# Kernel tuning notes

Measured on AMD Instinct MI355X. Metric: run time of the kernel, lower is better.

The kernel has to match this reference:

```python
import jax, jax.numpy as jnp
import numpy as np

S, B, D = 2048, 2, 768
H = 12
DK = D // H
DFF = 3072
EPS = 1e-5


def _layernorm(x, g, b):
    mu = jnp.mean(x, axis=-1, keepdims=True)
    var = jnp.mean(jnp.square(x - mu), axis=-1, keepdims=True)
    return (x - mu) * jax.lax.rsqrt(var + EPS) * g + b


def setup_inputs() -> dict:
    key = jax.random.key(0)
    ks = jax.random.split(key, 12)
    s = 0.02
    return {
        "x": jax.random.normal(ks[0], (S, B, D), jnp.float32),
        "wq": jax.random.normal(ks[1], (D, D), jnp.float32) * s,
        "bq": jnp.zeros((D,), jnp.float32),
        "wk": jax.random.normal(ks[2], (D, D), jnp.float32) * s,
        "bk": jnp.zeros((D,), jnp.float32),
        "wv": jax.random.normal(ks[3], (D, D), jnp.float32) * s,
        "bv": jnp.zeros((D,), jnp.float32),
        "wo": jax.random.normal(ks[4], (D, D), jnp.float32) * s,
        "bo": jnp.zeros((D,), jnp.float32),
        "g1": jnp.ones((D,), jnp.float32),
        "b1": jnp.zeros((D,), jnp.float32),
        "g2": jnp.ones((D,), jnp.float32),
        "b2": jnp.zeros((D,), jnp.float32),
        "w1": jax.random.normal(ks[5], (DFF, D), jnp.float32) * s,
        "bb1": jnp.zeros((DFF,), jnp.float32),
        "w2": jax.random.normal(ks[6], (D, DFF), jnp.float32) * s,
        "bb2": jnp.zeros((D,), jnp.float32),
    }


def reference(x, wq, bq, wk, bk, wv, bv, wo, bo, g1, b1, g2, b2, w1, bb1, w2, bb2):
    scale = 1.0 / np.sqrt(DK)
    # --- pre-norm MHA ---
    z = _layernorm(x, g1, b1)                      # [S,B,D]
    q = (z @ wq.T + bq).reshape(S, B, H, DK)
    k = (z @ wk.T + bk).reshape(S, B, H, DK)
    v = (z @ wv.T + bv).reshape(S, B, H, DK)
    scores = jnp.einsum('ibhd,jbhd->ijbh', q, k) * scale  # [S,S,B,H]
    attn = jax.nn.softmax(scores, axis=1)                  # softmax over keys
    ctx = jnp.einsum('ijbh,jbhd->ibhd', attn, v).reshape(S, B, D)
    a = ctx @ wo.T + bo
    x = x + a
    # --- pre-norm FFN (ELU) ---
    z = _layernorm(x, g2, b2)
    h = jax.nn.elu(z @ w1.T + bb1)
    a = h @ w2.T + bb2
    return x + a
```

## Files before the change

### kernel.cpp

```cpp
#include <hip/hip_runtime.h>
#include <hip/hip_bf16.h>
#include <math.h>

#define S_LEN   2048
#define B_SZ    2
#define D_MODEL 768
#define N_HEADS 12
#define DFF     3072
#define N_TOK   4096
#define EPS     1e-5f
#define QKV_N   2304
#define SLOG2E  0.18033688011112042f
#define NSPLIT  2
#define NTILE   (S_LEN / 64 / NSPLIT)

typedef __attribute__((ext_vector_type(8))) short short8;
typedef __attribute__((ext_vector_type(4))) float f32x4;
typedef unsigned long long u64;
typedef unsigned short u16;
typedef unsigned u32;

__device__ __forceinline__ void gload16(const void* g, void* l) {
    __builtin_amdgcn_global_load_lds(
        (const __attribute__((address_space(1))) void*)g,
        (__attribute__((address_space(3))) void*)l, 16, 0, 0);
}
__device__ __forceinline__ u16 f2bf(float x) {
    union { float f; unsigned u; } c; c.f = x;
    unsigned r = c.u + 0x7FFF + ((c.u >> 16) & 1);
    return (u16)(r >> 16);
}
__device__ __forceinline__ float bf2f(u16 u) {
    union { unsigned u; float f; } c; c.u = ((unsigned)u) << 16; return c.f;
}
__device__ __forceinline__ float fast_exp2(float x) {
    float r; asm("v_exp_f32 %0, %1" : "=v"(r) : "v"(x)); return r;
}

__global__ __launch_bounds__(256) void cvt_all(
    const float* __restrict__ wq, const float* __restrict__ wk,
    const float* __restrict__ wv, const float* __restrict__ wo,
    const float* __restrict__ w1, const float* __restrict__ w2,
    u16* __restrict__ dst)
{
    const int W = 147456;
    int i = blockIdx.x * 256 + threadIdx.x;
    const float* src; int off;
    if      (i <     W) { src = wq; off = 0;     }
    else if (i < 2 * W) { src = wk; off = W;     }
    else if (i < 3 * W) { src = wv; off = 2 * W; }
    else if (i < 4 * W) { src = wo; off = 3 * W; }
    else if (i < 8 * W) { src = w1; off = 4 * W; }
    else                { src = w2; off = 8 * W; }
    float4 v = ((const float4*)src)[i - off];
    union { u16 u[4]; u64 ll; } o;
    o.u[0] = f2bf(v.x); o.u[1] = f2bf(v.y); o.u[2] = f2bf(v.z); o.u[3] = f2bf(v.w);
    ((u64*)dst)[i] = o.ll;
}

__global__ __launch_bounds__(256) void concat_bias(
    const float* __restrict__ bq, const float* __restrict__ bk,
    const float* __restrict__ bv, float* __restrict__ d)
{
    int i = blockIdx.x * 256 + threadIdx.x;
    if (i < 768) d[i] = bq[i];
    else if (i < 1536) d[i] = bk[i - 768];
    else d[i] = bv[i - 1536];
}

__global__ __launch_bounds__(256) void ln_kernel(
    const float* __restrict__ x, const float* __restrict__ g,
    const float* __restrict__ b, u16* __restrict__ z)
{
    int row = blockIdx.x;
    const float* xr = x + (size_t)row * D_MODEL;
    u16* zr = z + (size_t)row * D_MODEL;
    int t = threadIdx.x;
    float loc[3];
    float s1 = 0.f, s2 = 0.f;
#pragma unroll
    for (int i = 0; i < 3; ++i) {
        float v = xr[t + 256 * i];
        loc[i] = v; s1 += v; s2 += v * v;
    }
#pragma unroll
    for (int off = 32; off > 0; off >>= 1) {
        s1 += __shfl_down(s1, off);
        s2 += __shfl_down(s2, off);
    }
    __shared__ float r1[4], r2[4];
    __shared__ float mu_s, is_s;
    int wave = t >> 6, lane = t & 63;
    if (lane == 0) { r1[wave] = s1; r2[wave] = s2; }
    __syncthreads();
    if (t == 0) {
        float a = r1[0] + r1[1] + r1[2] + r1[3];
        float c = r2[0] + r2[1] + r2[2] + r2[3];
        float mu = a * (1.f / D_MODEL);
        float var = c * (1.f / D_MODEL) - mu * mu;
        mu_s = mu; is_s = rsqrtf(var + EPS);
    }
    __syncthreads();
    float mu = mu_s, istd = is_s;
#pragma unroll
    for (int i = 0; i < 3; ++i) {
        int c = t + 256 * i;
        zr[c] = f2bf((loc[i] - mu) * istd * g[c] + b[c]);
    }
}

__global__ __launch_bounds__(256) void ln_fuse(
    const float* __restrict__ x, const u16* __restrict__ p0,
    const u16* __restrict__ p1, const float* __restrict__ bres,
    const float* __restrict__ g, const float* __restrict__ b,
    float* __restrict__ xout, u16* __restrict__ z)
{
    int row = blockIdx.x;
    const float* xr = x + (size_t)row * D_MODEL;
    const u16* p0r = p0 + (size_t)row * D_MODEL;
    const u16* p1r = p1 + (size_t)row * D_MODEL;
    int t = threadIdx.x;
    float loc[3];
    float s1 = 0.f, s2 = 0.f;
#pragma unroll
    for (int i = 0; i < 3; ++i) {
        int c = t + 256 * i;
        float v = xr[c] + bf2f(p0r[c]) + bf2f(p1r[c]) + bres[c];
        loc[i] = v; s1 += v; s2 += v * v;
    }
#pragma unroll
    for (int off = 32; off > 0; off >>= 1) {
        s1 += __shfl_down(s1, off);
        s2 += __shfl_down(s2, off);
    }
    __shared__ float r1[4], r2[4];
    __shared__ float mu_s, is_s;
    int wave = t >> 6, lane = t & 63;
    if (lane == 0) { r1[wave] = s1; r2[wave] = s2; }
    __syncthreads();
    if (t == 0) {
        float a = r1[0] + r1[1] + r1[2] + r1[3];
        float c = r2[0] + r2[1] + r2[2] + r2[3];
        float mu = a * (1.f / D_MODEL);
        float var = c * (1.f / D_MODEL) - mu * mu;
        mu_s = mu; is_s = rsqrtf(var + EPS);
    }
    __syncthreads();
    float mu = mu_s, istd = is_s;
    float* xo = xout + (size_t)row * D_MODEL;
    u16* zr = z + (size_t)row * D_MODEL;
#pragma unroll
    for (int i = 0; i < 3; ++i) {
        int c = t + 256 * i;
        xo[c] = loc[i];
        zr[c] = f2bf((loc[i] - mu) * istd * g[c] + b[c]);
    }
}

template <int MODE>
__global__ __launch_bounds__(256) void gemm_mfma(
    const u16* __restrict__ A, const u16* __restrict__ W,
    const float* __restrict__ bias, void* __restrict__ outp,
    u16* __restrict__ vt, int Ncols, int K, int lda, int ldw, int koff)
{
    __shared__ short AsB[3][128 * 32];
    __shared__ short BsB[3][128 * 32];

    const int t = threadIdx.x;
    const int lane = t & 63, w = t >> 6;
    const int wr = w >> 1, wc = w & 1;
    const int row0 = blockIdx.y * 128, col0 = blockIdx.x * 128;
    const int fr = lane & 15, fg = lane >> 4;

    if (MODE == 4) {
        A += (size_t)blockIdx.z * koff;
        W += (size_t)blockIdx.z * koff;
    }

    int o0 = w * 1024 + lane * 16;
    int r0s = o0 >> 6,          sl0 = (o0 >> 4) & 3;
    int r1s = (o0 + 4096) >> 6, sl1 = ((o0 + 4096) >> 4) & 3;
    int ss0 = sl0 ^ ((r0s >> 1) & 3);
    int ss1 = sl1 ^ ((r1s >> 1) & 3);
    const u16* Asrc0 = A + (size_t)(row0 + r0s) * lda + ss0 * 8;
    const u16* Asrc1 = A + (size_t)(row0 + r1s) * lda + ss1 * 8;
    const u16* Bsrc0 = W + (size_t)(col0 + r0s) * ldw + ss0 * 8;
    const u16* Bsrc1 = W + (size_t)(col0 + r1s) * ldw + ss1 * 8;
    const int od0 = w * 1024, od1 = w * 1024 + 4096;

    f32x4 acc[4][4] = {};
    const int nt = K / 32;

    auto stage = [&](int c, int k0) {
        gload16(Asrc0 + k0, (char*)AsB[c] + od0);
        gload16(Asrc1 + k0, (char*)AsB[c] + od1);
        gload16(Bsrc0 + k0, (char*)BsB[c] + od0);
        gload16(Bsrc1 + k0, (char*)BsB[c] + od1);
    };

    stage(0, 0);
    stage(1, 32);

    for (int tt = 0; tt < nt; ++tt) {
        if (tt + 1 < nt)
            asm volatile("s_waitcnt vmcnt(4)\n\ts_barrier" ::: "memory");
        else
            asm volatile("s_waitcnt vmcnt(0)\n\ts_barrier" ::: "memory");
        if (tt + 2 < nt) stage((tt + 2) % 3, (tt + 2) * 32);

        const char* As = (const char*)AsB[tt % 3];
        const char* Bs = (const char*)BsB[tt % 3];
        short8 af[4], bfr[4];
#pragma unroll
        for (int m = 0; m < 4; ++m) {
            int r = wr * 64 + m * 16 + fr;
            af[m] = *(const short8*)(As + r * 64 + ((fg ^ ((r >> 1) & 3)) << 4));
        }
#pragma unroll
        for (int n = 0; n < 4; ++n) {
            int r = wc * 64 + n * 16 + fr;
            bfr[n] = *(const short8*)(Bs + r * 64 + ((fg ^ ((r >> 1) & 3)) << 4));
        }
#pragma unroll
        for (int m = 0; m < 4; ++m)
#pragma unroll
            for (int n = 0; n < 4; ++n)
                acc[m][n] = __builtin_amdgcn_mfma_f32_16x16x32_bf16(
                    af[m], bfr[n], acc[m][n], 0, 0, 0);
    }

    u16* pout16 = nullptr;
    if (MODE == 4) pout16 = blockIdx.z ? vt : (u16*)outp;

#pragma unroll
    for (int m = 0; m < 4; ++m) {
        int rbase = row0 + wr * 64 + m * 16 + fg * 4;
#pragma unroll
        for (int n = 0; n < 4; ++n) {
            int col = col0 + wc * 64 + n * 16 + fr;
            float bv = (MODE == 4) ? 0.f : bias[col];
            if (MODE == 1 && col >= 1536) {
                int cc = col - 1536, hh = cc >> 6, dk = cc & 63;
                int s_a = rbase >> 1;
                float v0 = acc[m][n][0] + bv, v1 = acc[m][n][1] + bv;
                float v2 = acc[m][n][2] + bv, v3 = acc[m][n][3] + bv;
                unsigned lo = (unsigned)f2bf(v0) | ((unsigned)f2bf(v2) << 16);
                unsigned hi = (unsigned)f2bf(v1) | ((unsigned)f2bf(v3) << 16);
                *(unsigned*)&vt[((size_t)hh * 64 + dk) * 2048 + s_a] = lo;
                *(unsigned*)&vt[((size_t)(N_HEADS + hh) * 64 + dk) * 2048 + s_a] = hi;
            } else {
#pragma unroll
                for (int r = 0; r < 4; ++r) {
                    int row = rbase + r;
                    float v = acc[m][n][r] + bv;
                    if (MODE == 3) {
                        v = v > 0.f ? v : (fast_exp2(v * 1.44269504f) - 1.f);
                        ((u16*)outp)[(size_t)row * Ncols + col] = f2bf(v);
                    } else if (MODE == 4) {
                        pout16[(size_t)row * 768 + col] = f2bf(v);
                    } else {
                        if (col < 768) v *= SLOG2E;
                        ((u16*)outp)[(size_t)row * QKV_N + col] = f2bf(v);
                    }
                }
            }
        }
    }
}

__global__ __launch_bounds__(256) void reduce_add(
    const u16* __restrict__ p0, const u16* __restrict__ p1,
    const float* __restrict__ bias, const float* __restrict__ res,
    float* __restrict__ out)
{
    int i = blockIdx.x * 256 + threadIdx.x;
    int col4 = i % (D_MODEL / 4);
    u64 a = ((const u64*)p0)[i];
    u64 c = ((const u64*)p1)[i];
    float4 o = ((const float4*)res)[i];
    float4 bb = ((const float4*)bias)[col4];
    o.x += bf2f((u16)a)         + bf2f((u16)c)         + bb.x;
    o.y += bf2f((u16)(a >> 16)) + bf2f((u16)(c >> 16)) + bb.y;
    o.z += bf2f((u16)(a >> 32)) + bf2f((u16)(c >> 32)) + bb.z;
    o.w += bf2f((u16)(a >> 48)) + bf2f((u16)(c >> 48)) + bb.w;
    ((float4*)out)[i] = o;
}

__global__ __launch_bounds__(256) void attn_mfma(
    const u16* qkv, const u16* __restrict__ vt,
    u16* op0, u16* __restrict__ op1, float2* __restrict__ mlp)
{
    __shared__ short KsB[2][64 * 64];
    __shared__ short VtB[2][64 * 64];
    __shared__ short PsB[4][16 * 64];

    const int t = threadIdx.x, lane = t & 63, w = t >> 6;
    const int fr = lane & 15, fg = lane >> 4;
    const int fg4 = fg * 4;
    const int qb = blockIdx.x, bh = blockIdx.y, zid = blockIdx.z;
    const int b = bh / N_HEADS, h = bh % N_HEADS;

    short8 qf[2];
    {
        int srow = qb * 64 + w * 16 + fr;
        size_t tok = (size_t)srow * B_SZ + b;
#pragma unroll
        for (int s = 0; s < 2; ++s)
            qf[s] = *(const short8*)(qkv + tok * QKV_N + h * 64 + s * 32 + fg * 8);
    }

    const short8 ones8 = { (short)0x3F80, (short)0x3F80, (short)0x3F80, (short)0x3F80,
                           (short)0x3F80, (short)0x3F80, (short)0x3F80, (short)0x3F80 };

    float m2 = -1e30f;
    f32x4 l_acc = {};
    f32x4 O[4] = {};

    int o0 = w * 1024 + lane * 16;
    int r0 = o0 >> 7,          sl0 = (o0 >> 4) & 7;
    int r1 = (o0 + 4096) >> 7, sl1 = ((o0 + 4096) >> 4) & 7;
    int ss0 = sl0 ^ (r0 & 7), ss1 = sl1 ^ (r1 & 7);
    const u16* kbase = qkv + 768 + h * 64;
    const u16* vtb = vt + (size_t)bh * 64 * S_LEN;
    const int od0 = w * 1024, od1 = w * 1024 + 4096;
    char* Pw = (char*)PsB[w];

    auto stageKV = [&](int c, int kb) {
        gload16(kbase + ((size_t)(kb * 64 + r0) * B_SZ + b) * QKV_N + ss0 * 8, (char*)KsB[c] + od0);
        gload16(kbase + ((size_t)(kb * 64 + r1) * B_SZ + b) * QKV_N + ss1 * 8, (char*)KsB[c] + od1);
        gload16(vtb + (size_t)r0 * S_LEN + kb * 64 + ss0 * 8, (char*)VtB[c] + od0);
        gload16(vtb + (size_t)r1 * S_LEN + kb * 64 + ss1 * 8, (char*)VtB[c] + od1);
    };

    const int kb0 = zid * NTILE;
    stageKV(0, kb0);

    for (int it = 0; it < NTILE; ++it) {
        __syncthreads();
        if (it + 1 < NTILE) stageKV((it + 1) & 1, kb0 + it + 1);
        const char* Ks  = (const char*)KsB[it & 1];
        const char* Vts = (const char*)VtB[it & 1];

        f32x4 sacc[4] = {};
        __builtin_amdgcn_s_setprio(1);
#pragma unroll
        for (int f = 0; f < 4; ++f) {
            int r = f * 16 + fr;
#pragma unroll
            for (int s = 0; s < 2; ++s) {
                int slot = (s * 4 + fg) ^ (r & 7);
                short8 kf = *(const short8*)(Ks + r * 128 + slot * 16);
                sacc[f] = __builtin_amdgcn_mfma_f32_16x16x32_bf16(kf, qf[s], sacc[f], 0, 0, 0);
            }
        }
        __builtin_amdgcn_s_setprio(0);

        float p[16];
        float mx = -1e30f;
#pragma unroll
        for (int f = 0; f < 4; ++f)
#pragma unroll
            for (int r = 0; r < 4; ++r) {
                float vv = sacc[f][r];
                p[f * 4 + r] = vv;
                mx = fmaxf(mx, vv);
            }
        mx = fmaxf(mx, __shfl_xor(mx, 16));
        mx = fmaxf(mx, __shfl_xor(mx, 32));

        if (!__all(mx - m2 <= 8.f)) {
            float mnew = fmaxf(m2, mx);
            float alpha = fast_exp2(m2 - mnew);
            m2 = mnew;
            float a0 = __shfl(alpha, fg4 + 0), a1 = __shfl(alpha, fg4 + 1);
            float a2 = __shfl(alpha, fg4 + 2), a3 = __shfl(alpha, fg4 + 3);
#pragma unroll
            for (int n = 0; n < 4; ++n) {
                O[n][0] *= a0; O[n][1] *= a1; O[n][2] *= a2; O[n][3] *= a3;
            }
            l_acc[0] *= a0; l_acc[1] *= a1; l_acc[2] *= a2; l_acc[3] *= a3;
        }

#pragma unroll
        for (int i = 0; i < 16; ++i)
            p[i] = fast_exp2(p[i] - m2);

#pragma unroll
        for (int f = 0; f < 4; ++f) {
            u32 u0, u1;
            asm("v_cvt_pk_bf16_f32 %0, %1, %2" : "=v"(u0) : "v"(p[4 * f + 0]), "v"(p[4 * f + 1]));
            asm("v_cvt_pk_bf16_f32 %0, %1, %2" : "=v"(u1) : "v"(p[4 * f + 2]), "v"(p[4 * f + 3]));
            int slot = (f * 2 + (fg >> 1)) ^ (fr & 7);
            uint2 uu; uu.x = u0; uu.y = u1;
            *(uint2*)(Pw + fr * 128 + slot * 16 + (fg & 1) * 8) = uu;
        }
        asm volatile("s_waitcnt lgkmcnt(0)" ::: "memory");
        __builtin_amdgcn_sched_barrier(0);

        __builtin_amdgcn_s_setprio(1);
#pragma unroll
        for (int s = 0; s < 2; ++s) {
            int pslot = (s * 4 + fg) ^ (fr & 7);
            short8 pf = *(const short8*)(Pw + fr * 128 + pslot * 16);
            l_acc = __builtin_amdgcn_mfma_f32_16x16x32_bf16(pf, ones8, l_acc, 0, 0, 0);
#pragma unroll
            for (int n = 0; n < 4; ++n) {
                int vrow = n * 16 + fr;
                int vslot = (s * 4 + fg) ^ (vrow & 7);
                short8 vf = *(const short8*)(Vts + vrow * 128 + vslot * 16);
                O[n] = __builtin_amdgcn_mfma_f32_16x16x32_bf16(pf, vf, O[n], 0, 0, 0);
            }
        }
        __builtin_amdgcn_s_setprio(0);
    }

    float mm0 = __shfl(m2, fg4 + 0), mm1 = __shfl(m2, fg4 + 1);
    float mm2 = __shfl(m2, fg4 + 2), mm3 = __shfl(m2, fg4 + 3);
    int srow = qb * 64 + w * 16 + fg4;
    size_t tok0 = (size_t)srow * B_SZ + b;
    u16* op = zid ? op1 : op0;
    const int ld = zid ? 768 : QKV_N;
#pragma unroll
    for (int n = 0; n < 4; ++n) {
        int col = h * 64 + n * 16 + fr;
        op[(tok0 + 0) * ld + col] = f2bf(O[n][0]);
        op[(tok0 + 2) * ld + col] = f2bf(O[n][1]);
        op[(tok0 + 4) * ld + col] = f2bf(O[n][2]);
        op[(tok0 + 6) * ld + col] = f2bf(O[n][3]);
    }
    if (fr == 0) {
        float2* mlz = mlp + (size_t)zid * (N_TOK * N_HEADS);
        mlz[(tok0 + 0) * N_HEADS + h] = make_float2(mm0, l_acc[0]);
        mlz[(tok0 + 2) * N_HEADS + h] = make_float2(mm1, l_acc[1]);
        mlz[(tok0 + 4) * N_HEADS + h] = make_float2(mm2, l_acc[2]);
        mlz[(tok0 + 6) * N_HEADS + h] = make_float2(mm3, l_acc[3]);
    }
}

__global__ __launch_bounds__(256) void combine_attn(
    const u16* __restrict__ op0, const u16* op1,
    const float2* __restrict__ ml, u16* ctx)
{
    int i = blockIdx.x * 256 + threadIdx.x;
    int tok = i / 192, c4 = i % 192, h = c4 >> 4;
    float2 q0 = ml[tok * N_HEADS + h];
    float2 q1 = ml[N_TOK * N_HEADS + tok * N_HEADS + h];
    float m = fmaxf(q0.x, q1.x);
    float a0 = fast_exp2(q0.x - m), a1 = fast_exp2(q1.x - m);
    float inv = 1.f / (a0 * q0.y + a1 * q1.y);
    a0 *= inv; a1 *= inv;
    u64 o0 = *(const u64*)(op0 + (size_t)tok * QKV_N + c4 * 4);
    u64 o1 = *(const u64*)(op1 + (size_t)tok * 768 + c4 * 4);
    union { u16 u[4]; u64 ll; } r;
#pragma unroll
    for (int j = 0; j < 4; ++j)
        r.u[j] = f2bf(a0 * bf2f((u16)(o0 >> (16 * j))) +
                      a1 * bf2f((u16)(o1 >> (16 * j))));
    *(u64*)(ctx + (size_t)tok * 768 + c4 * 4) = r.ll;
}

extern "C" void kernel_launch(void* const* d_in, const int* in_sizes, int n_in,
                              void* d_out, int out_size, void* d_ws, size_t ws_size,
                              hipStream_t stream)
{
    (void)in_sizes; (void)n_in; (void)out_size; (void)ws_size;
    const float* x   = (const float*)d_in[0];
    const float* wq  = (const float*)d_in[1];
    const float* bq  = (const float*)d_in[2];
    const float* wk  = (const float*)d_in[3];
    const float* bk  = (const float*)d_in[4];
    const float* wv  = (const float*)d_in[5];
    const float* bv  = (const float*)d_in[6];
    const float* wo  = (const float*)d_in[7];
    const float* bo  = (const float*)d_in[8];
    const float* g1  = (const float*)d_in[9];
    const float* b1  = (const float*)d_in[10];
    const float* g2  = (const float*)d_in[11];
    const float* b2  = (const float*)d_in[12];
    const float* w1  = (const float*)d_in[13];
    const float* bb1 = (const float*)d_in[14];
    const float* w2  = (const float*)d_in[15];
    const float* bb2 = (const float*)d_in[16];
    float* out = (float*)d_out;

    const size_t ND = (size_t)N_TOK * D_MODEL;
    char* p = (char*)d_ws;
    u16* z    = (u16*)p;
    p += ND * 2;
    u16* qkv  = (u16*)p;
    u16* hbuf = (u16*)p;
    p += (size_t)N_TOK * QKV_N * 2;
    u16* vtb  = (u16*)p;
    p += (size_t)B_SZ * N_HEADS * 64 * S_LEN * 2;
    u16* wqkvb = (u16*)p;
    p += (size_t)QKV_N * D_MODEL * 2;
    u16* wob   = (u16*)p; p += (size_t)D_MODEL * D_MODEL * 2;
    u16* w1b   = (u16*)p; p += (size_t)DFF * D_MODEL * 2;
    u16* w2b   = (u16*)p; p += (size_t)D_MODEL * DFF * 2;
    float* biasqkv = (float*)p;

    u16* aop0 = qkv + 1536;
    u16* aop1 = z;
    float2* aml = (float2*)wqkvb;
    u16* wop0 = qkv;
    u16* wop1 = qkv + ND;
    u16* fp0  = z;
    u16* fp1  = wqkvb;

    dim3 blk(256);

    cvt_all<<<6912, blk, 0, stream>>>(wq, wk, wv, wo, w1, w2, wqkvb);
    concat_bias<<<9, blk, 0, stream>>>(bq, bk, bv, biasqkv);

    ln_kernel<<<N_TOK, blk, 0, stream>>>(x, g1, b1, z);
    gemm_mfma<1><<<dim3(QKV_N / 128, N_TOK / 128), blk, 0, stream>>>(
        z, wqkvb, biasqkv, qkv, vtb, QKV_N, D_MODEL, D_MODEL, D_MODEL, 0);
    attn_mfma<<<dim3(S_LEN / 64, B_SZ * N_HEADS, NSPLIT), blk, 0, stream>>>(
        qkv, vtb, aop0, aop1, aml);
    combine_attn<<<(int)(ND / 4 / 256), blk, 0, stream>>>(aop0, aop1, aml, z);
    gemm_mfma<4><<<dim3(D_MODEL / 128, N_TOK / 128, 2), blk, 0, stream>>>(
        z, wob, nullptr, wop0, wop1, D_MODEL, 384, D_MODEL, D_MODEL, 384);
    ln_fuse<<<N_TOK, blk, 0, stream>>>(x, wop0, wop1, bo, g2, b2, out, z);
    gemm_mfma<3><<<dim3(DFF / 128, N_TOK / 128), blk, 0, stream>>>(
        z, w1b, bb1, hbuf, nullptr, DFF, D_MODEL, D_MODEL, D_MODEL, 0);
    gemm_mfma<4><<<dim3(D_MODEL / 128, N_TOK / 128, 2), blk, 0, stream>>>(
        hbuf, w2b, nullptr, fp0, fp1, D_MODEL, 1536, DFF, DFF, 1536);
    reduce_add<<<(int)(ND / 4 / 256), blk, 0, stream>>>(fp0, fp1, bb2, out, out);
}
```

Measured before the change: 202.5 us.

## Use two-wave GEMM blocks with 64x128 per-wave tiles

The MFMA GEMM moves from four waves covering 64x64 each to two waves covering 64x128 each of the same 128x128 block tile. Each wave now reuses its A fragments across 8 B fragments, which raises MFMA work per LDS read, and each thread issues 8 global-to-LDS loads per stage instead of 4. The cost is half as many waves per block for hiding latency and twice the accumulator registers (128 floats), which may lower occupancy or cause spills.

```diff
diff --git a/kernel.cpp b/kernel.cpp
--- a/kernel.cpp
+++ b/kernel.cpp
@@ -158,7 +158,7 @@
 }
 
 template <int MODE>
-__global__ __launch_bounds__(256) void gemm_mfma(
+__global__ __launch_bounds__(128) void gemm_mfma(
     const u16* __restrict__ A, const u16* __restrict__ W,
     const float* __restrict__ bias, void* __restrict__ outp,
     u16* __restrict__ vt, int Ncols, int K, int lda, int ldw, int koff)
@@ -168,7 +168,6 @@
 
     const int t = threadIdx.x;
     const int lane = t & 63, w = t >> 6;
-    const int wr = w >> 1, wc = w & 1;
     const int row0 = blockIdx.y * 128, col0 = blockIdx.x * 128;
     const int fr = lane & 15, fg = lane >> 4;
 
@@ -177,25 +176,31 @@
         W += (size_t)blockIdx.z * koff;
     }
 
-    int o0 = w * 1024 + lane * 16;
-    int r0s = o0 >> 6,          sl0 = (o0 >> 4) & 3;
-    int r1s = (o0 + 4096) >> 6, sl1 = ((o0 + 4096) >> 4) & 3;
-    int ss0 = sl0 ^ ((r0s >> 1) & 3);
-    int ss1 = sl1 ^ ((r1s >> 1) & 3);
-    const u16* Asrc0 = A + (size_t)(row0 + r0s) * lda + ss0 * 8;
-    const u16* Asrc1 = A + (size_t)(row0 + r1s) * lda + ss1 * 8;
-    const u16* Bsrc0 = W + (size_t)(col0 + r0s) * ldw + ss0 * 8;
-    const u16* Bsrc1 = W + (size_t)(col0 + r1s) * ldw + ss1 * 8;
-    const int od0 = w * 1024, od1 = w * 1024 + 4096;
-
-    f32x4 acc[4][4] = {};
+    int rs[4], ssl[4];
+#pragma unroll
+    for (int j = 0; j < 4; ++j) {
+        int o = j * 2048 + t * 16;
+        rs[j] = o >> 6;
+        int sl = (o >> 4) & 3;
+        ssl[j] = sl ^ ((rs[j] >> 1) & 3);
+    }
+    const u16* Asrc[4]; const u16* Bsrc[4];
+#pragma unroll
+    for (int j = 0; j < 4; ++j) {
+        Asrc[j] = A + (size_t)(row0 + rs[j]) * lda + ssl[j] * 8;
+        Bsrc[j] = W + (size_t)(col0 + rs[j]) * ldw + ssl[j] * 8;
+    }
+
+    f32x4 acc[4][8] = {};
     const int nt = K / 32;
 
     auto stage = [&](int c, int k0) {
-        gload16(Asrc0 + k0, (char*)AsB[c] + od0);
-        gload16(Asrc1 + k0, (char*)AsB[c] + od1);
-        gload16(Bsrc0 + k0, (char*)BsB[c] + od0);
-        gload16(Bsrc1 + k0, (char*)BsB[c] + od1);
+#pragma unroll
+        for (int j = 0; j < 4; ++j)
+            gload16(Asrc[j] + k0, (char*)AsB[c] + j * 2048 + t * 16);
+#pragma unroll
+        for (int j = 0; j < 4; ++j)
+            gload16(Bsrc[j] + k0, (char*)BsB[c] + j * 2048 + t * 16);
     };
 
     stage(0, 0);
@@ -203,28 +208,28 @@
 
     for (int tt = 0; tt < nt; ++tt) {
         if (tt + 1 < nt)
-            asm volatile("s_waitcnt vmcnt(4)\n\ts_barrier" ::: "memory");
+            asm volatile("s_waitcnt vmcnt(8)\n\ts_barrier" ::: "memory");
         else
             asm volatile("s_waitcnt vmcnt(0)\n\ts_barrier" ::: "memory");
         if (tt + 2 < nt) stage((tt + 2) % 3, (tt + 2) * 32);
 
         const char* As = (const char*)AsB[tt % 3];
         const char* Bs = (const char*)BsB[tt % 3];
-        short8 af[4], bfr[4];
+        short8 af[4], bfr[8];
 #pragma unroll
         for (int m = 0; m < 4; ++m) {
-            int r = wr * 64 + m * 16 + fr;
+            int r = w * 64 + m * 16 + fr;
             af[m] = *(const short8*)(As + r * 64 + ((fg ^ ((r >> 1) & 3)) << 4));
         }
 #pragma unroll
-        for (int n = 0; n < 4; ++n) {
-            int r = wc * 64 + n * 16 + fr;
+        for (int n = 0; n < 8; ++n) {
+            int r = n * 16 + fr;
             bfr[n] = *(const short8*)(Bs + r * 64 + ((fg ^ ((r >> 1) & 3)) << 4));
         }
 #pragma unroll
         for (int m = 0; m < 4; ++m)
 #pragma unroll
-            for (int n = 0; n < 4; ++n)
+            for (int n = 0; n < 8; ++n)
                 acc[m][n] = __builtin_amdgcn_mfma_f32_16x16x32_bf16(
                     af[m], bfr[n], acc[m][n], 0, 0, 0);
     }
@@ -234,10 +239,10 @@
 
 #pragma unroll
     for (int m = 0; m < 4; ++m) {
-        int rbase = row0 + wr * 64 + m * 16 + fg * 4;
-#pragma unroll
-        for (int n = 0; n < 4; ++n) {
-            int col = col0 + wc * 64 + n * 16 + fr;
+        int rbase = row0 + w * 64 + m * 16 + fg * 4;
+#pragma unroll
+        for (int n = 0; n < 8; ++n) {
+            int col = col0 + n * 16 + fr;
             float bv = (MODE == 4) ? 0.f : bias[col];
             if (MODE == 1 && col >= 1536) {
                 int cc = col - 1536, hh = cc >> 6, dk = cc & 63;
@@ -508,22 +513,23 @@
     u16* fp1  = wqkvb;
 
     dim3 blk(256);
+    dim3 blkg(128);
 
     cvt_all<<<6912, blk, 0, stream>>>(wq, wk, wv, wo, w1, w2, wqkvb);
     concat_bias<<<9, blk, 0, stream>>>(bq, bk, bv, biasqkv);
 
     ln_kernel<<<N_TOK, blk, 0, stream>>>(x, g1, b1, z);
-    gemm_mfma<1><<<dim3(QKV_N / 128, N_TOK / 128), blk, 0, stream>>>(
+    gemm_mfma<1><<<dim3(QKV_N / 128, N_TOK / 128), blkg, 0, stream>>>(
         z, wqkvb, biasqkv, qkv, vtb, QKV_N, D_MODEL, D_MODEL, D_MODEL, 0);
     attn_mfma<<<dim3(S_LEN / 64, B_SZ * N_HEADS, NSPLIT), blk, 0, stream>>>(
         qkv, vtb, aop0, aop1, aml);
     combine_attn<<<(int)(ND / 4 / 256), blk, 0, stream>>>(aop0, aop1, aml, z);
-    gemm_mfma<4><<<dim3(D_MODEL / 128, N_TOK / 128, 2), blk, 0, stream>>>(
+    gemm_mfma<4><<<dim3(D_MODEL / 128, N_TOK / 128, 2), blkg, 0, stream>>>(
         z, wob, nullptr, wop0, wop1, D_MODEL, 384, D_MODEL, D_MODEL, 384);
     ln_fuse<<<N_TOK, blk, 0, stream>>>(x, wop0, wop1, bo, g2, b2, out, z);
-    gemm_mfma<3><<<dim3(DFF / 128, N_TOK / 128), blk, 0, stream>>>(
+    gemm_mfma<3><<<dim3(DFF / 128, N_TOK / 128), blkg, 0, stream>>>(
         z, w1b, bb1, hbuf, nullptr, DFF, D_MODEL, D_MODEL, D_MODEL, 0);
-    gemm_mfma<4><<<dim3(D_MODEL / 128, N_TOK / 128, 2), blk, 0, stream>>>(
+    gemm_mfma<4><<<dim3(D_MODEL / 128, N_TOK / 128, 2), blkg, 0, stream>>>(
         hbuf, w2b, nullptr, fp0, fp1, D_MODEL, 1536, DFF, DFF, 1536);
     reduce_add<<<(int)(ND / 4 / 256), blk, 0, stream>>>(fp0, fp1, bb2, out, out);
 }
```

Result: slower. 260.2 us (+28.5%).
